# Kernel optimization log

Measured on AMD Instinct MI355X. Metric: run time of the kernel, lower is better.

The kernel has to match this reference:

```python
import jax, jax.numpy as jnp
import numpy as np

B, N, E, F, U = 256, 240, 4338, 28, 100
NEG_SLOPE = 0.2  # PyG GATConv default negative_slope


def setup_inputs() -> dict:
    key = jax.random.key(0)
    ks = jax.random.split(key, 13)
    s = 0.05  # xavier-ish scale
    return {
        "inputs": jax.random.normal(ks[0], (B, N * F), jnp.float32),
        "state": jax.random.normal(ks[1], (B, N * U), jnp.float32),
        "edge_src": jax.random.randint(ks[2], (E,), 0, N, jnp.int32),
        "edge_dst": jax.random.randint(ks[3], (E,), 0, N, jnp.int32),
        # GATConv(U+F -> U): linear weight, attention vectors, output bias
        "Wg": jax.random.normal(ks[4], (U, U + F), jnp.float32) * s,
        "att_src": jax.random.normal(ks[5], (U,), jnp.float32) * s,
        "att_dst": jax.random.normal(ks[6], (U,), jnp.float32) * s,
        "gat_bias": jnp.zeros((U,), jnp.float32),
        # bias_1 added in _gc3 (self.biases[(100,)])
        "bias1": jnp.zeros((U,), jnp.float32),
        # GRU1: GRULinear(100, 200); GRU2: GRULinear(100, 100)
        "W_ru": jax.random.normal(ks[7], (U + F, 2 * U), jnp.float32) * s,
        "b_ru": jnp.zeros((2 * U,), jnp.float32),
        "W_c": jax.random.normal(ks[8], (U + F, U), jnp.float32) * s,
        "b_c": jnp.zeros((U,), jnp.float32),
    }


def _gat_gru(inputs, state, src, dst, Wg, att_src, att_dst, gat_bias, bias1,
             W_ru, b_ru, W_c, b_c):
    xi = inputs.reshape(B, N, F)
    xs = state.reshape(B, N, U)
    # _gc3: concat [state, inputs] -> GATConv per sample (vectorized here)
    x = jnp.concatenate([xs, xi], axis=2)                 # [B, N, U+F]
    h = jnp.einsum("bnf,cf->bnc", x, Wg)                  # [B, N, U]
    a_src = h @ att_src                                    # [B, N]
    a_dst = h @ att_dst                                    # [B, N]
    e = jax.nn.leaky_relu(a_src[:, src] + a_dst[:, dst], NEG_SLOPE)  # [B, E+N]
    eT = e.T                                               # [E+N, B]
    emax = jax.ops.segment_max(eT, dst, num_segments=N)    # [N, B]
    ex = jnp.exp(eT - emax[dst])
    denom = jax.ops.segment_sum(ex, dst, num_segments=N)   # [N, B]
    alpha = ex / denom[dst]                                # [E+N, B]
    msgs = h[:, src].transpose(1, 0, 2) * alpha[:, :, None]  # [E+N, B, U]
    agg = jax.ops.segment_sum(msgs, dst, num_segments=N)   # [N, B, U]
    gstate = agg.transpose(1, 0, 2) + gat_bias + bias1     # [B, N, U]
    st = gstate.reshape(B, N * U)
    # GRU gates (GRULinear concatenates [inputs, hidden] on feature dim)
    cat1 = jnp.concatenate([xi, gstate], axis=2).reshape(-1, U + F)
    ru = jax.nn.sigmoid((cat1 @ W_ru + b_ru).reshape(B, N, 2 * U))
    r = ru[..., :U].reshape(B, N * U)
    u = ru[..., U:].reshape(B, N * U)
    cat2 = jnp.concatenate([xi, (r * st).reshape(B, N, U)], axis=2).reshape(-1, U + F)
    c = jnp.tanh(cat2 @ W_c + b_c).reshape(B, N * U)
    return u * st + (1.0 - u) * c


def reference(inputs, state, edge_src, edge_dst, Wg, att_src, att_dst,
              gat_bias, bias1, W_ru, b_ru, W_c, b_c):
    # PyG GATConv default add_self_loops=True
    loops = jnp.arange(N, dtype=edge_src.dtype)
    src = jnp.concatenate([edge_src, loops])
    dst = jnp.concatenate([edge_dst, loops])
    return _gat_gru(inputs, state, src, dst, Wg, att_src, att_dst, gat_bias,
                    bias1, W_ru, b_ru, W_c, b_c)
```

## Files before the change

### kernel.cpp

```cpp
#include <hip/hip_runtime.h>

#define Bb 256
#define Nn 240
#define Ee 4338
#define Ff 28
#define Uu 100
#define Kk 128
#define Mrows (Bb * Nn)
#define ET (Ee + Nn)
#define AS 136

typedef __attribute__((ext_vector_type(8))) short bf16x8;
typedef __attribute__((ext_vector_type(4))) float f32x4;
typedef unsigned short u16;

__device__ __forceinline__ float bf2f(u16 u) {
  union { unsigned int i; float f; } v; v.i = ((unsigned int)u) << 16; return v.f;
}
__device__ __forceinline__ u16 f2bf(float f) {
  union { float ff; unsigned int i; } v; v.ff = f;
  unsigned int x = v.i;
  return (u16)((x + 0x7fffu + ((x >> 16) & 1u)) >> 16);
}
__device__ __forceinline__ void split4(const float4 v, ushort4& h, ushort4& l) {
  u16 h0 = f2bf(v.x), h1 = f2bf(v.y), h2 = f2bf(v.z), h3 = f2bf(v.w);
  h.x = h0; h.y = h1; h.z = h2; h.w = h3;
  l.x = f2bf(v.x - bf2f(h0)); l.y = f2bf(v.y - bf2f(h1));
  l.z = f2bf(v.z - bf2f(h2)); l.w = f2bf(v.w - bf2f(h3));
}

__global__ __launch_bounds__(256) void k_prep(
    const float* __restrict__ Wg, const float* __restrict__ Wru, const float* __restrict__ Wc,
    u16* __restrict__ wgh, u16* __restrict__ wgl,
    u16* __restrict__ wruh, u16* __restrict__ wrul,
    u16* __restrict__ wch, u16* __restrict__ wcl) {
  int gt = blockIdx.x * 256 + threadIdx.x, GS = gridDim.x * 256;
  for (int i = gt; i < 128 * Kk; i += GS) {
    int c = i >> 7, k = i & 127;
    float v = (c < Uu) ? Wg[c * Kk + k] : 0.f;
    u16 h = f2bf(v); wgh[i] = h; wgl[i] = f2bf(v - bf2f(h));
  }
  for (int i = gt; i < 256 * Kk; i += GS) {
    int n = i >> 7, kp = i & 127;
    int k = (kp < Uu) ? (kp + Ff) : (kp - Uu);
    float v = (n < 2 * Uu) ? Wru[k * (2 * Uu) + n] : 0.f;
    u16 h = f2bf(v); wruh[i] = h; wrul[i] = f2bf(v - bf2f(h));
  }
  for (int i = gt; i < 128 * Kk; i += GS) {
    int n = i >> 7, kp = i & 127;
    int k = (kp < Uu) ? (kp + Ff) : (kp - Uu);
    float v = (n < Uu) ? Wc[k * Uu + n] : 0.f;
    u16 h = f2bf(v); wch[i] = h; wcl[i] = f2bf(v - bf2f(h));
  }
}

__global__ __launch_bounds__(256) void k_csr(
    const int* __restrict__ esrc, const int* __restrict__ edst,
    int* __restrict__ coff, int* __restrict__ cslot) {
  __shared__ int cnt[Nn];
  __shared__ int offs[Nn + 1];
  __shared__ int cur[Nn];
  int tid = threadIdx.x;
  for (int n = tid; n < Nn; n += 256) cnt[n] = 0;
  __syncthreads();
  for (int e = tid; e < Ee; e += 256) atomicAdd(&cnt[edst[e]], 1);
  __syncthreads();
  if (tid == 0) {
    int run = 0;
    for (int n = 0; n < Nn; ++n) { offs[n] = run; run += cnt[n] + 1; }
    offs[Nn] = run;
  }
  __syncthreads();
  for (int n = tid; n < Nn; n += 256) cur[n] = offs[n];
  for (int n = tid; n <= Nn; n += 256) coff[n] = offs[n];
  __syncthreads();
  for (int e = tid; e < Ee; e += 256) {
    int d = edst[e];
    cslot[atomicAdd(&cur[d], 1)] = esrc[e];
  }
  for (int n = tid; n < Nn; n += 256) cslot[atomicAdd(&cur[n], 1)] = n;
}

__global__ __launch_bounds__(256, 4) void k_gemm1(
    const float* __restrict__ stt, const float* __restrict__ inp,
    const u16* __restrict__ wgh, const u16* __restrict__ wgl,
    const float* __restrict__ att_s, const float* __restrict__ att_d,
    float* __restrict__ h, float* __restrict__ asrc, float* __restrict__ adst) {
  __shared__ u16 ahL[32 * AS];
  __shared__ u16 alL[32 * AS];
  __shared__ float sredA[32], sredD[32];
  int tid = threadIdx.x;
  int m0 = blockIdx.x * 32;
  if (tid < 32) sredA[tid] = 0.f;
  else if (tid < 64) sredD[tid - 32] = 0.f;
  for (int j = tid; j < 32 * 32; j += 256) {
    int r = j >> 5, g = j & 31;
    float4 v = (g < 25) ? *(const float4*)(stt + (size_t)(m0 + r) * Uu + g * 4)
                        : *(const float4*)(inp + (size_t)(m0 + r) * Ff + (g - 25) * 4);
    ushort4 hh, ll;
    split4(v, hh, ll);
    *(ushort4*)(ahL + r * AS + g * 4) = hh;
    *(ushort4*)(alL + r * AS + g * 4) = ll;
  }
  __syncthreads();

  int w = tid >> 6, l = tid & 63, l15 = l & 15, q = l >> 4;
  f32x4 zero = {0.f, 0.f, 0.f, 0.f};
  float sa[8] = {0.f, 0.f, 0.f, 0.f, 0.f, 0.f, 0.f, 0.f};
  float sd[8] = {0.f, 0.f, 0.f, 0.f, 0.f, 0.f, 0.f, 0.f};

#pragma unroll
  for (int pass = 0; pass < 2; ++pass) {
    int T = pass * 4 + w;
    bf16x8 wh[4], wl[4];
#pragma unroll
    for (int s = 0; s < 4; ++s) {
      const int o = (T * 16 + l15) * Kk + s * 32 + q * 8;
      wh[s] = *(const bf16x8*)(wgh + o);
      wl[s] = *(const bf16x8*)(wgl + o);
    }
    f32x4 acc[2];
    acc[0] = zero; acc[1] = zero;
#pragma unroll
    for (int rt = 0; rt < 2; ++rt) {
#pragma unroll
      for (int s = 0; s < 4; ++s) {
        bf16x8 a = *(const bf16x8*)(ahL + (rt * 16 + l15) * AS + s * 32 + q * 8);
        bf16x8 b = *(const bf16x8*)(alL + (rt * 16 + l15) * AS + s * 32 + q * 8);
        acc[rt] = __builtin_amdgcn_mfma_f32_16x16x32_bf16(a, wh[s], acc[rt], 0, 0, 0);
        acc[rt] = __builtin_amdgcn_mfma_f32_16x16x32_bf16(b, wh[s], acc[rt], 0, 0, 0);
        acc[rt] = __builtin_amdgcn_mfma_f32_16x16x32_bf16(a, wl[s], acc[rt], 0, 0, 0);
      }
    }
    int c = T * 16 + l15;
    float av = (c < Uu) ? att_s[c] : 0.f, dv = (c < Uu) ? att_d[c] : 0.f;
#pragma unroll
    for (int rt = 0; rt < 2; ++rt) {
#pragma unroll
      for (int i = 0; i < 4; ++i) {
        float v = acc[rt][i];
        int row = rt * 16 + q * 4 + i;
        if (c < Uu) h[(size_t)(m0 + row) * Uu + c] = v;
        sa[rt * 4 + i] += v * av;
        sd[rt * 4 + i] += v * dv;
      }
    }
  }
#pragma unroll
  for (int rt = 0; rt < 2; ++rt) {
#pragma unroll
    for (int i = 0; i < 4; ++i) {
      float va = sa[rt * 4 + i], vd = sd[rt * 4 + i];
#pragma unroll
      for (int msk = 1; msk < 16; msk <<= 1) {
        va += __shfl_xor(va, msk, 64);
        vd += __shfl_xor(vd, msk, 64);
      }
      int row = rt * 16 + q * 4 + i;
      if (l15 == 0) {
        atomicAdd(&sredA[row], va);
        atomicAdd(&sredD[row], vd);
      }
    }
  }
  __syncthreads();
  if (tid < 32) {
    asrc[m0 + tid] = sredA[tid];
    adst[m0 + tid] = sredD[tid];
  }
}

__global__ __launch_bounds__(256) void k_attn(
    const int* __restrict__ coff, const int* __restrict__ cslot,
    const float* __restrict__ asrc, const float* __restrict__ adst,
    const float* __restrict__ h, const float* __restrict__ gbias, const float* __restrict__ b1,
    float* __restrict__ gsf) {
  int b = blockIdx.x;
  int w = threadIdx.x >> 6, lane = threadIdx.x & 63;
  int n = blockIdx.y * 4 + w;
  int o0 = coff[n], deg = coff[n + 1] - o0;
  float ad = adst[b * Nn + n];
  const float* hb = h + (size_t)b * Nn * Uu;
  int half = lane >> 5, ll = lane & 31;
  bool act = (ll < 25);

  float ax = 0.f, ay = 0.f, az = 0.f, aw = 0.f;
  float den = 0.f;
  for (int c0 = 0; c0 < deg; c0 += 64) {
    int e = c0 + lane;
    float we = 0.f; int s = 0;
    if (e < deg) {
      s = cslot[o0 + e];
      float sc = asrc[b * Nn + s] + ad;
      sc = (sc > 0.f) ? sc : 0.2f * sc;
      we = __expf(sc);
    }
    float d = we;
#pragma unroll
    for (int msk = 1; msk < 64; msk <<= 1) d += __shfl_xor(d, msk, 64);
    den += d;

    int cn = (deg - c0 < 64) ? (deg - c0) : 64;
    for (int e2 = 0; e2 < cn; e2 += 2) {
      int eh = e2 + half;
      float w2 = __shfl(we, eh, 64);
      int s2 = __shfl(s, eh, 64);
      if (act && eh < cn) {
        const float4 hv = *(const float4*)(hb + (size_t)s2 * Uu + ll * 4);
        ax += w2 * hv.x; ay += w2 * hv.y; az += w2 * hv.z; aw += w2 * hv.w;
      }
    }
  }
  ax += __shfl_xor(ax, 32, 64);
  ay += __shfl_xor(ay, 32, 64);
  az += __shfl_xor(az, 32, 64);
  aw += __shfl_xor(aw, 32, 64);
  if (lane < 25) {
    float inv = 1.f / den;
    int u0 = lane * 4;
    float4 o;
    o.x = ax * inv + gbias[u0 + 0] + b1[u0 + 0];
    o.y = ay * inv + gbias[u0 + 1] + b1[u0 + 1];
    o.z = az * inv + gbias[u0 + 2] + b1[u0 + 2];
    o.w = aw * inv + gbias[u0 + 3] + b1[u0 + 3];
    *(float4*)(gsf + ((size_t)b * Nn + n) * Uu + u0) = o;
  }
}

__global__ __launch_bounds__(256, 4) void k_gru(
    const float* __restrict__ gsf, const float* __restrict__ inp,
    const u16* __restrict__ wruh, const u16* __restrict__ wrul,
    const float* __restrict__ bru,
    const u16* __restrict__ wch, const u16* __restrict__ wcl,
    const float* __restrict__ bc,
    float* __restrict__ out) {
  __shared__ u16 ahL[32 * AS];
  __shared__ u16 alL[32 * AS];
  __shared__ u16 ugQ[32 * Uu];
  int tid = threadIdx.x;
  int m0 = blockIdx.x * 32;
  for (int j = tid; j < 32 * 32; j += 256) {
    int r = j >> 5, g = j & 31;
    float4 v = (g < 25) ? *(const float4*)(gsf + (size_t)(m0 + r) * Uu + g * 4)
                        : *(const float4*)(inp + (size_t)(m0 + r) * Ff + (g - 25) * 4);
    ushort4 hh, ll;
    split4(v, hh, ll);
    *(ushort4*)(ahL + r * AS + g * 4) = hh;
    *(ushort4*)(alL + r * AS + g * 4) = ll;
  }

  int w = tid >> 6, l = tid & 63, l15 = l & 15, q = l >> 4;
  int c0p = w * 16 + l15, c1p = (w + 4) * 16 + l15;

  float sv[2][2][4];
#pragma unroll
  for (int rt = 0; rt < 2; ++rt) {
#pragma unroll
    for (int i = 0; i < 4; ++i) {
      int row = rt * 16 + q * 4 + i;
#pragma unroll
      for (int t = 0; t < 2; ++t) {
        int c = t ? c1p : c0p;
        sv[t][rt][i] = (c < Uu) ? gsf[(size_t)(m0 + row) * Uu + c] : 0.f;
      }
    }
  }
  __syncthreads();

  f32x4 zero = {0.f, 0.f, 0.f, 0.f};
  float pr[2][2][4];

#pragma unroll
  for (int pass = 0; pass < 4; ++pass) {
    int T = pass * 4 + w;
    bf16x8 wh[4], wl[4];
#pragma unroll
    for (int s = 0; s < 4; ++s) {
      const int o = (T * 16 + l15) * Kk + s * 32 + q * 8;
      wh[s] = *(const bf16x8*)(wruh + o);
      wl[s] = *(const bf16x8*)(wrul + o);
    }
    f32x4 acc[2];
    acc[0] = zero; acc[1] = zero;
#pragma unroll
    for (int rt = 0; rt < 2; ++rt) {
#pragma unroll
      for (int s = 0; s < 4; ++s) {
        bf16x8 a = *(const bf16x8*)(ahL + (rt * 16 + l15) * AS + s * 32 + q * 8);
        bf16x8 b = *(const bf16x8*)(alL + (rt * 16 + l15) * AS + s * 32 + q * 8);
        acc[rt] = __builtin_amdgcn_mfma_f32_16x16x32_bf16(a, wh[s], acc[rt], 0, 0, 0);
        acc[rt] = __builtin_amdgcn_mfma_f32_16x16x32_bf16(b, wh[s], acc[rt], 0, 0, 0);
        acc[rt] = __builtin_amdgcn_mfma_f32_16x16x32_bf16(a, wl[s], acc[rt], 0, 0, 0);
      }
    }
    int c = T * 16 + l15;
    float bv = (c < 2 * Uu) ? bru[c] : 0.f;
#pragma unroll
    for (int rt = 0; rt < 2; ++rt) {
#pragma unroll
      for (int i = 0; i < 4; ++i) {
        int row = rt * 16 + q * 4 + i;
        float y = acc[rt][i] + bv;
        float g = 1.f / (1.f + __expf(-y));
        if (pass < 2) {
          if (c < Uu) pr[pass][rt][i] = g * sv[pass][rt][i];
        }
        if (c >= Uu && c < 2 * Uu) {
          ugQ[row * Uu + (c - Uu)] = (u16)(g * 65535.f + 0.5f);
        }
      }
    }
  }

  __syncthreads();
#pragma unroll
  for (int rt = 0; rt < 2; ++rt) {
#pragma unroll
    for (int i = 0; i < 4; ++i) {
      int row = rt * 16 + q * 4 + i;
#pragma unroll
      for (int t = 0; t < 2; ++t) {
        int c = t ? c1p : c0p;
        if (c < Uu) {
          float p = pr[t][rt][i];
          u16 hh = f2bf(p);
          ahL[row * AS + c] = hh;
          alL[row * AS + c] = f2bf(p - bf2f(hh));
        }
      }
    }
  }
  __syncthreads();

#pragma unroll
  for (int t = 0; t < 2; ++t) {
    int T = t * 4 + w;
    bf16x8 wh[4], wl[4];
#pragma unroll
    for (int s = 0; s < 4; ++s) {
      const int o = (T * 16 + l15) * Kk + s * 32 + q * 8;
      wh[s] = *(const bf16x8*)(wch + o);
      wl[s] = *(const bf16x8*)(wcl + o);
    }
    f32x4 acc[2];
    acc[0] = zero; acc[1] = zero;
#pragma unroll
    for (int rt = 0; rt < 2; ++rt) {
#pragma unroll
      for (int s = 0; s < 4; ++s) {
        bf16x8 a = *(const bf16x8*)(ahL + (rt * 16 + l15) * AS + s * 32 + q * 8);
        bf16x8 b = *(const bf16x8*)(alL + (rt * 16 + l15) * AS + s * 32 + q * 8);
        acc[rt] = __builtin_amdgcn_mfma_f32_16x16x32_bf16(a, wh[s], acc[rt], 0, 0, 0);
        acc[rt] = __builtin_amdgcn_mfma_f32_16x16x32_bf16(b, wh[s], acc[rt], 0, 0, 0);
        acc[rt] = __builtin_amdgcn_mfma_f32_16x16x32_bf16(a, wl[s], acc[rt], 0, 0, 0);
      }
    }
    int c = t ? c1p : c0p;
    float bv = (c < Uu) ? bc[c] : 0.f;
#pragma unroll
    for (int rt = 0; rt < 2; ++rt) {
#pragma unroll
      for (int i = 0; i < 4; ++i) {
        int row = rt * 16 + q * 4 + i;
        size_t m = (size_t)(m0 + row);
        if (c < Uu) {
          float y = acc[rt][i] + bv;
          float cv = 1.f - 2.f / (__expf(2.f * y) + 1.f);
          float u = (float)ugQ[row * Uu + c] * (1.f / 65535.f);
          out[m * Uu + c] = u * sv[t][rt][i] + (1.f - u) * cv;
        }
      }
    }
  }
}

extern "C" void kernel_launch(void* const* d_in, const int* in_sizes, int n_in,
                              void* d_out, int out_size, void* d_ws, size_t ws_size,
                              hipStream_t stream) {
  const float* inp   = (const float*)d_in[0];
  const float* stt   = (const float*)d_in[1];
  const int*   esrc  = (const int*)d_in[2];
  const int*   edst  = (const int*)d_in[3];
  const float* Wg    = (const float*)d_in[4];
  const float* att_s = (const float*)d_in[5];
  const float* att_d = (const float*)d_in[6];
  const float* gbias = (const float*)d_in[7];
  const float* b1    = (const float*)d_in[8];
  const float* Wru   = (const float*)d_in[9];
  const float* bru   = (const float*)d_in[10];
  const float* Wc    = (const float*)d_in[11];
  const float* bc    = (const float*)d_in[12];
  float* out = (float*)d_out;

  char* base = (char*)d_ws;
  size_t o = 0;
  auto alloc = [&](size_t bytes) -> void* {
    void* p = base + o;
    o = (o + bytes + 255) & ~(size_t)255;
    return p;
  };
  u16* wgh  = (u16*)alloc(128 * Kk * sizeof(u16));
  u16* wgl  = (u16*)alloc(128 * Kk * sizeof(u16));
  u16* wruh = (u16*)alloc(256 * Kk * sizeof(u16));
  u16* wrul = (u16*)alloc(256 * Kk * sizeof(u16));
  u16* wch  = (u16*)alloc(128 * Kk * sizeof(u16));
  u16* wcl  = (u16*)alloc(128 * Kk * sizeof(u16));
  int* coff  = (int*)alloc((Nn + 1) * sizeof(int));
  int* cslot = (int*)alloc(ET * sizeof(int));
  float* h    = (float*)alloc((size_t)Mrows * Uu * sizeof(float));
  float* asrc = (float*)alloc((size_t)Mrows * sizeof(float));
  float* adst = (float*)alloc((size_t)Mrows * sizeof(float));
  float* gsf  = (float*)alloc((size_t)Mrows * Uu * sizeof(float));

  k_prep<<<32, 256, 0, stream>>>(Wg, Wru, Wc, wgh, wgl, wruh, wrul, wch, wcl);
  k_csr<<<1, 256, 0, stream>>>(esrc, edst, coff, cslot);
  k_gemm1<<<Mrows / 32, 256, 0, stream>>>(stt, inp, wgh, wgl, att_s, att_d, h, asrc, adst);
  k_attn<<<dim3(Bb, 60), 256, 0, stream>>>(coff, cslot, asrc, adst, h, gbias, b1, gsf);
  k_gru<<<Mrows / 32, 256, 0, stream>>>(gsf, inp, wruh, wrul, bru, wch, wcl, bc, out);
}
```

Before: 241.9 us.

## Double GEMM block width to 8 waves and parallelize CSR offset scan

The GEMM and GRU kernels now launch 512 threads per block, so each of 8 waves owns one 16-column tile instead of looping over two or four tiles per wave. This cuts the serial MFMA work per wave and register pressure, and raises wave-level parallelism per block. The CSR builder replaces its single-thread serial prefix sum with a shared-memory Hillis-Steele block scan. The trade-off is more waves contending for the same LDS tile and extra barriers in the scan.

```diff
diff --git a/kernel.cpp b/kernel.cpp
--- a/kernel.cpp
+++ b/kernel.cpp
@@ -57,22 +57,29 @@
 __global__ __launch_bounds__(256) void k_csr(
     const int* __restrict__ esrc, const int* __restrict__ edst,
     int* __restrict__ coff, int* __restrict__ cslot) {
-  __shared__ int cnt[Nn];
-  __shared__ int offs[Nn + 1];
+  __shared__ int cnt[256];
+  __shared__ int scan[256];
   __shared__ int cur[Nn];
   int tid = threadIdx.x;
-  for (int n = tid; n < Nn; n += 256) cnt[n] = 0;
+  cnt[tid] = 0;
   __syncthreads();
   for (int e = tid; e < Ee; e += 256) atomicAdd(&cnt[edst[e]], 1);
   __syncthreads();
-  if (tid == 0) {
-    int run = 0;
-    for (int n = 0; n < Nn; ++n) { offs[n] = run; run += cnt[n] + 1; }
-    offs[Nn] = run;
-  }
-  __syncthreads();
-  for (int n = tid; n < Nn; n += 256) cur[n] = offs[n];
-  for (int n = tid; n <= Nn; n += 256) coff[n] = offs[n];
+  int x = (tid < Nn) ? (cnt[tid] + 1) : 0;
+  int incl = x;
+  scan[tid] = incl;
+  __syncthreads();
+#pragma unroll
+  for (int d = 1; d < 256; d <<= 1) {
+    int t = (tid >= d) ? scan[tid - d] : 0;
+    __syncthreads();
+    incl += t;
+    scan[tid] = incl;
+    __syncthreads();
+  }
+  int excl = incl - x;
+  if (tid < Nn) { coff[tid] = excl; cur[tid] = excl; }
+  if (tid == 0) coff[Nn] = scan[Nn - 1];
   __syncthreads();
   for (int e = tid; e < Ee; e += 256) {
     int d = edst[e];
@@ -81,7 +88,7 @@
   for (int n = tid; n < Nn; n += 256) cslot[atomicAdd(&cur[n], 1)] = n;
 }
 
-__global__ __launch_bounds__(256, 4) void k_gemm1(
+__global__ __launch_bounds__(512, 8) void k_gemm1(
     const float* __restrict__ stt, const float* __restrict__ inp,
     const u16* __restrict__ wgh, const u16* __restrict__ wgl,
     const float* __restrict__ att_s, const float* __restrict__ att_d,
@@ -93,7 +100,7 @@
   int m0 = blockIdx.x * 32;
   if (tid < 32) sredA[tid] = 0.f;
   else if (tid < 64) sredD[tid - 32] = 0.f;
-  for (int j = tid; j < 32 * 32; j += 256) {
+  for (int j = tid; j < 32 * 32; j += 512) {
     int r = j >> 5, g = j & 31;
     float4 v = (g < 25) ? *(const float4*)(stt + (size_t)(m0 + r) * Uu + g * 4)
                         : *(const float4*)(inp + (size_t)(m0 + r) * Ff + (g - 25) * 4);
@@ -106,57 +113,43 @@
 
   int w = tid >> 6, l = tid & 63, l15 = l & 15, q = l >> 4;
   f32x4 zero = {0.f, 0.f, 0.f, 0.f};
-  float sa[8] = {0.f, 0.f, 0.f, 0.f, 0.f, 0.f, 0.f, 0.f};
-  float sd[8] = {0.f, 0.f, 0.f, 0.f, 0.f, 0.f, 0.f, 0.f};
-
-#pragma unroll
-  for (int pass = 0; pass < 2; ++pass) {
-    int T = pass * 4 + w;
-    bf16x8 wh[4], wl[4];
+
+  int T = w;
+  bf16x8 wh[4], wl[4];
+#pragma unroll
+  for (int s = 0; s < 4; ++s) {
+    const int o = (T * 16 + l15) * Kk + s * 32 + q * 8;
+    wh[s] = *(const bf16x8*)(wgh + o);
+    wl[s] = *(const bf16x8*)(wgl + o);
+  }
+  f32x4 acc[2];
+  acc[0] = zero; acc[1] = zero;
+#pragma unroll
+  for (int rt = 0; rt < 2; ++rt) {
 #pragma unroll
     for (int s = 0; s < 4; ++s) {
-      const int o = (T * 16 + l15) * Kk + s * 32 + q * 8;
-      wh[s] = *(const bf16x8*)(wgh + o);
-      wl[s] = *(const bf16x8*)(wgl + o);
-    }
-    f32x4 acc[2];
-    acc[0] = zero; acc[1] = zero;
-#pragma unroll
-    for (int rt = 0; rt < 2; ++rt) {
-#pragma unroll
-      for (int s = 0; s < 4; ++s) {
-        bf16x8 a = *(const bf16x8*)(ahL + (rt * 16 + l15) * AS + s * 32 + q * 8);
-        bf16x8 b = *(const bf16x8*)(alL + (rt * 16 + l15) * AS + s * 32 + q * 8);
-        acc[rt] = __builtin_amdgcn_mfma_f32_16x16x32_bf16(a, wh[s], acc[rt], 0, 0, 0);
-        acc[rt] = __builtin_amdgcn_mfma_f32_16x16x32_bf16(b, wh[s], acc[rt], 0, 0, 0);
-        acc[rt] = __builtin_amdgcn_mfma_f32_16x16x32_bf16(a, wl[s], acc[rt], 0, 0, 0);
-      }
-    }
-    int c = T * 16 + l15;
-    float av = (c < Uu) ? att_s[c] : 0.f, dv = (c < Uu) ? att_d[c] : 0.f;
-#pragma unroll
-    for (int rt = 0; rt < 2; ++rt) {
-#pragma unroll
-      for (int i = 0; i < 4; ++i) {
-        float v = acc[rt][i];
-        int row = rt * 16 + q * 4 + i;
-        if (c < Uu) h[(size_t)(m0 + row) * Uu + c] = v;
-        sa[rt * 4 + i] += v * av;
-        sd[rt * 4 + i] += v * dv;
-      }
-    }
-  }
+      bf16x8 a = *(const bf16x8*)(ahL + (rt * 16 + l15) * AS + s * 32 + q * 8);
+      bf16x8 b = *(const bf16x8*)(alL + (rt * 16 + l15) * AS + s * 32 + q * 8);
+      acc[rt] = __builtin_amdgcn_mfma_f32_16x16x32_bf16(a, wh[s], acc[rt], 0, 0, 0);
+      acc[rt] = __builtin_amdgcn_mfma_f32_16x16x32_bf16(b, wh[s], acc[rt], 0, 0, 0);
+      acc[rt] = __builtin_amdgcn_mfma_f32_16x16x32_bf16(a, wl[s], acc[rt], 0, 0, 0);
+    }
+  }
+  int c = T * 16 + l15;
+  float av = (c < Uu) ? att_s[c] : 0.f, dv = (c < Uu) ? att_d[c] : 0.f;
 #pragma unroll
   for (int rt = 0; rt < 2; ++rt) {
 #pragma unroll
     for (int i = 0; i < 4; ++i) {
-      float va = sa[rt * 4 + i], vd = sd[rt * 4 + i];
+      float v = acc[rt][i];
+      int row = rt * 16 + q * 4 + i;
+      if (c < Uu) h[(size_t)(m0 + row) * Uu + c] = v;
+      float va = v * av, vd = v * dv;
 #pragma unroll
       for (int msk = 1; msk < 16; msk <<= 1) {
         va += __shfl_xor(va, msk, 64);
         vd += __shfl_xor(vd, msk, 64);
       }
-      int row = rt * 16 + q * 4 + i;
       if (l15 == 0) {
         atomicAdd(&sredA[row], va);
         atomicAdd(&sredD[row], vd);
@@ -227,7 +220,7 @@
   }
 }
 
-__global__ __launch_bounds__(256, 4) void k_gru(
+__global__ __launch_bounds__(512, 8) void k_gru(
     const float* __restrict__ gsf, const float* __restrict__ inp,
     const u16* __restrict__ wruh, const u16* __restrict__ wrul,
     const float* __restrict__ bru,
@@ -239,7 +232,7 @@
   __shared__ u16 ugQ[32 * Uu];
   int tid = threadIdx.x;
   int m0 = blockIdx.x * 32;
-  for (int j = tid; j < 32 * 32; j += 256) {
+  for (int j = tid; j < 32 * 32; j += 512) {
     int r = j >> 5, g = j & 31;
     float4 v = (g < 25) ? *(const float4*)(gsf + (size_t)(m0 + r) * Uu + g * 4)
                         : *(const float4*)(inp + (size_t)(m0 + r) * Ff + (g - 25) * 4);
@@ -250,29 +243,25 @@
   }
 
   int w = tid >> 6, l = tid & 63, l15 = l & 15, q = l >> 4;
-  int c0p = w * 16 + l15, c1p = (w + 4) * 16 + l15;
-
-  float sv[2][2][4];
+  int cw = w * 16 + l15;
+
+  float sv[2][4];
 #pragma unroll
   for (int rt = 0; rt < 2; ++rt) {
 #pragma unroll
     for (int i = 0; i < 4; ++i) {
       int row = rt * 16 + q * 4 + i;
-#pragma unroll
-      for (int t = 0; t < 2; ++t) {
-        int c = t ? c1p : c0p;
-        sv[t][rt][i] = (c < Uu) ? gsf[(size_t)(m0 + row) * Uu + c] : 0.f;
-      }
+      sv[rt][i] = (cw < Uu) ? gsf[(size_t)(m0 + row) * Uu + cw] : 0.f;
     }
   }
   __syncthreads();
 
   f32x4 zero = {0.f, 0.f, 0.f, 0.f};
-  float pr[2][2][4];
-
-#pragma unroll
-  for (int pass = 0; pass < 4; ++pass) {
-    int T = pass * 4 + w;
+  float pr[2][4];
+
+#pragma unroll
+  for (int pass = 0; pass < 2; ++pass) {
+    int T = pass * 8 + w;
     bf16x8 wh[4], wl[4];
 #pragma unroll
     for (int s = 0; s < 4; ++s) {
@@ -302,9 +291,7 @@
         int row = rt * 16 + q * 4 + i;
         float y = acc[rt][i] + bv;
         float g = 1.f / (1.f + __expf(-y));
-        if (pass < 2) {
-          if (c < Uu) pr[pass][rt][i] = g * sv[pass][rt][i];
-        }
+        if (pass == 0 && c < Uu) pr[rt][i] = g * sv[rt][i];
         if (c >= Uu && c < 2 * Uu) {
           ugQ[row * Uu + (c - Uu)] = (u16)(g * 65535.f + 0.5f);
         }
@@ -318,23 +305,18 @@
 #pragma unroll
     for (int i = 0; i < 4; ++i) {
       int row = rt * 16 + q * 4 + i;
-#pragma unroll
-      for (int t = 0; t < 2; ++t) {
-        int c = t ? c1p : c0p;
-        if (c < Uu) {
-          float p = pr[t][rt][i];
-          u16 hh = f2bf(p);
-          ahL[row * AS + c] = hh;
-          alL[row * AS + c] = f2bf(p - bf2f(hh));
-        }
-      }
-    }
-  }
-  __syncthreads();
-
-#pragma unroll
-  for (int t = 0; t < 2; ++t) {
-    int T = t * 4 + w;
+      if (cw < Uu) {
+        float p = pr[rt][i];
+        u16 hh = f2bf(p);
+        ahL[row * AS + cw] = hh;
+        alL[row * AS + cw] = f2bf(p - bf2f(hh));
+      }
+    }
+  }
+  __syncthreads();
+
+  {
+    int T = w;
     bf16x8 wh[4], wl[4];
 #pragma unroll
     for (int s = 0; s < 4; ++s) {
@@ -355,19 +337,18 @@
         acc[rt] = __builtin_amdgcn_mfma_f32_16x16x32_bf16(a, wl[s], acc[rt], 0, 0, 0);
       }
     }
-    int c = t ? c1p : c0p;
+    int c = cw;
     float bv = (c < Uu) ? bc[c] : 0.f;
 #pragma unroll
     for (int rt = 0; rt < 2; ++rt) {
 #pragma unroll
       for (int i = 0; i < 4; ++i) {
         int row = rt * 16 + q * 4 + i;
-        size_t m = (size_t)(m0 + row);
         if (c < Uu) {
           float y = acc[rt][i] + bv;
           float cv = 1.f - 2.f / (__expf(2.f * y) + 1.f);
           float u = (float)ugQ[row * Uu + c] * (1.f / 65535.f);
-          out[m * Uu + c] = u * sv[t][rt][i] + (1.f - u) * cv;
+          out[(size_t)(m0 + row) * Uu + c] = u * sv[rt][i] + (1.f - u) * cv;
         }
       }
     }
@@ -414,7 +395,7 @@
 
   k_prep<<<32, 256, 0, stream>>>(Wg, Wru, Wc, wgh, wgl, wruh, wrul, wch, wcl);
   k_csr<<<1, 256, 0, stream>>>(esrc, edst, coff, cslot);
-  k_gemm1<<<Mrows / 32, 256, 0, stream>>>(stt, inp, wgh, wgl, att_s, att_d, h, asrc, adst);
+  k_gemm1<<<Mrows / 32, 512, 0, stream>>>(stt, inp, wgh, wgl, att_s, att_d, h, asrc, adst);
   k_attn<<<dim3(Bb, 60), 256, 0, stream>>>(coff, cslot, asrc, adst, h, gbias, b1, gsf);
-  k_gru<<<Mrows / 32, 256, 0, stream>>>(gsf, inp, wruh, wrul, bru, wch, wcl, bc, out);
-}
+  k_gru<<<Mrows / 32, 512, 0, stream>>>(gsf, inp, wruh, wrul, bru, wch, wcl, bc, out);
+}
```

Result: slower. 281.3 us (+16.3%).
